# Optimization experiments

Hardware: AMD Instinct MI355X
Metric: run time of the kernel (lower is better)

Reference implementation:

```python
import jax, jax.numpy as jnp
import numpy as np

DIM = 256
NUM_HEADS = 8
SCALE = (DIM // NUM_HEADS) ** -0.5  # matches torch: head_dim**-0.5, even though no head split happens
THRESH = 0.6


def setup_inputs() -> dict:
    key = jax.random.key(0)
    ks = jax.random.split(key, 6)
    B, N = 4, 4096
    x = jax.random.normal(ks[0], (B, N, DIM), dtype=jnp.float32)
    y = jax.random.normal(ks[1], (B, N, DIM), dtype=jnp.float32)
    s = DIM ** -0.5
    Wq = jax.random.normal(ks[2], (DIM, DIM), dtype=jnp.float32) * s
    Wk = jax.random.normal(ks[3], (DIM, DIM), dtype=jnp.float32) * s
    Wv = jax.random.normal(ks[4], (DIM, DIM), dtype=jnp.float32) * s
    Wp = jax.random.normal(ks[5], (DIM, DIM), dtype=jnp.float32) * s
    bp = jnp.zeros((DIM,), dtype=jnp.float32)
    return {"x": x, "y": y, "Wq": Wq, "Wk": Wk, "Wv": Wv, "Wp": Wp, "bp": bp}


def reference(x, y, Wq, Wk, Wv, Wp, bp):
    # q,v from x; k from y (cross attention, no head split — faithful to source)
    q = jnp.einsum('bnd,de->bne', x, Wq)
    k = jnp.einsum('bnd,de->bne', y, Wk)
    v = jnp.einsum('bnd,de->bne', x, Wv)
    attn = jnp.einsum('bnd,bmd->bnm', q, k) * SCALE  # [B, N, N]
    attn = jax.nn.softmax(attn, axis=-1)
    attn = jnp.where(attn < THRESH, jnp.zeros((), attn.dtype), attn)  # hard threshold
    out = jnp.einsum('bnm,bmd->bnd', attn, v)
    out = jnp.einsum('bnd,de->bne', out, Wp) + bp
    return out
```

## Files before the change

### kernel.cpp

```cpp
#include <hip/hip_runtime.h>
#include <cstdint>
#include <cmath>

#define DIM     256
#define NSEQ    4096
#define SCALE   0.17677669529663687f
#define THRESH  0.6f
#define BAND    0.01f
#define MAXSUSP 8000
#define NCHUNK  32
#define C1      0.2550349f
#define C2      28.8539008f

using half8 = __attribute__((ext_vector_type(8))) _Float16;
using half4 = __attribute__((ext_vector_type(4))) _Float16;
using f32x4 = __attribute__((ext_vector_type(4))) float;

__device__ __forceinline__ void async_copy16(const void* gsrc, void* ldst) {
    __builtin_amdgcn_global_load_lds(
        (const __attribute__((address_space(1))) void*)gsrc,
        (__attribute__((address_space(3))) void*)ldst, 16, 0, 0);
}

__global__ void prep_kernel(const float* __restrict__ W0, const float* __restrict__ W1,
                            const float* __restrict__ W2, const float* __restrict__ W3,
                            float* __restrict__ Wt, _Float16* __restrict__ Wth,
                            int* __restrict__ susp)
{
    __shared__ float tile[64][68];
    int t = threadIdx.x;
    int m = blockIdx.x >> 4;
    int ti = blockIdx.x & 15;
    int tr = (ti >> 2) * 64, tc = (ti & 3) * 64;
    const float* W = (m == 0) ? W0 : (m == 1) ? W1 : (m == 2) ? W2 : W3;
    if (blockIdx.x == 0 && t < 2) susp[t] = 0;
    int rr = t >> 4, c4 = (t & 15) * 4;
#pragma unroll
    for (int p = 0; p < 4; ++p) {
        int row = p * 16 + rr;
        *(float4*)&tile[row][c4] = *(const float4*)(W + (size_t)(tr + row) * DIM + tc + c4);
    }
    __syncthreads();
#pragma unroll
    for (int p = 0; p < 4; ++p) {
        int c = p * 16 + rr;
        float4 v;
        v.x = tile[c4 + 0][c]; v.y = tile[c4 + 1][c];
        v.z = tile[c4 + 2][c]; v.w = tile[c4 + 3][c];
        size_t ot = (size_t)(tc + c) * DIM + tr + c4;
        if (m == 0) *(float4*)(Wt + ot) = v;
        half4 hv;
        hv[0] = (_Float16)v.x; hv[1] = (_Float16)v.y;
        hv[2] = (_Float16)v.z; hv[3] = (_Float16)v.w;
        *(half4*)(Wth + (size_t)m * 65536 + ot) = hv;
    }
}

__global__ __launch_bounds__(256, 2)
void proj3_mfma(const float* __restrict__ x, const float* __restrict__ y,
                const _Float16* __restrict__ Wth,
                _Float16* __restrict__ qh, _Float16* __restrict__ kh,
                float* __restrict__ kf, _Float16* __restrict__ vh)
{
    __shared__ half8 sA[1024];
    __shared__ half8 sB[1024];
    int tid = threadIdx.x, w = tid >> 6, ln = tid & 63;
    int rb = blockIdx.x * 128, cb = blockIdx.y * 128, m = blockIdx.z;
    const float* A = (m == 1) ? y : x;
    const _Float16* B = Wth + (size_t)m * 65536;

    f32x4 acc[2][8];
#pragma unroll
    for (int mi = 0; mi < 2; ++mi)
#pragma unroll
        for (int nt = 0; nt < 8; ++nt) acc[mi][nt] = (f32x4){0.f, 0.f, 0.f, 0.f};

    int r = tid >> 1;
    int chalf = (tid & 1) * 4;
    for (int kc = 0; kc < 4; ++kc) {
        __syncthreads();
        const float*    asrc = A + (size_t)(rb + r) * DIM + kc * 64 + chalf * 8;
        const _Float16* bsrc = B + (size_t)(cb + r) * DIM + kc * 64 + chalf * 8;
#pragma unroll
        for (int cc = 0; cc < 4; ++cc) {
            int c = chalf + cc;
            float4 f0 = *(const float4*)(asrc + cc * 8);
            float4 f1 = *(const float4*)(asrc + cc * 8 + 4);
            half8 hv;
            hv[0] = (_Float16)f0.x; hv[1] = (_Float16)f0.y; hv[2] = (_Float16)f0.z; hv[3] = (_Float16)f0.w;
            hv[4] = (_Float16)f1.x; hv[5] = (_Float16)f1.y; hv[6] = (_Float16)f1.z; hv[7] = (_Float16)f1.w;
            int li = ((r >> 4) * 2 + (c >> 2)) * 64 + ((c & 3) << 4) + (r & 15);
            sA[li] = hv;
            sB[li] = *(const half8*)(bsrc + cc * 8);
        }
        __syncthreads();
#pragma unroll
        for (int s = 0; s < 2; ++s) {
            half8 a0 = sA[((w * 2 + 0) * 2 + s) * 64 + ln];
            half8 a1 = sA[((w * 2 + 1) * 2 + s) * 64 + ln];
#pragma unroll
            for (int nt = 0; nt < 8; ++nt) {
                half8 bv = sB[(nt * 2 + s) * 64 + ln];
                acc[0][nt] = __builtin_amdgcn_mfma_f32_16x16x32_f16(a0, bv, acc[0][nt], 0, 0, 0);
                acc[1][nt] = __builtin_amdgcn_mfma_f32_16x16x32_f16(a1, bv, acc[1][nt], 0, 0, 0);
            }
        }
    }
    int quad = ln >> 4, cix = ln & 15;
#pragma unroll
    for (int mi = 0; mi < 2; ++mi)
#pragma unroll
        for (int nt = 0; nt < 8; ++nt)
#pragma unroll
            for (int rr = 0; rr < 4; ++rr) {
                int row = rb + (w * 2 + mi) * 16 + quad * 4 + rr;
                int col = cb + nt * 16 + cix;
                size_t off = (size_t)row * DIM + col;
                float vv = acc[mi][nt][rr];
                if (m == 0)      qh[off] = (_Float16)vv;
                else if (m == 1) { kh[off] = (_Float16)vv; kf[off] = vv; }
                else             vh[off] = (_Float16)vv;
            }
}

__global__ __launch_bounds__(256, 2)
void flash_fp16(const _Float16* __restrict__ qh, const _Float16* __restrict__ kh,
                float* __restrict__ pm, float* __restrict__ pl, int* __restrict__ pam)
{
    __shared__ half8 sK[4096];
    int tid = threadIdx.x, w = tid >> 6, ln = tid & 63;
    int g = blockIdx.x;
    int qt = blockIdx.y;
    int ms = g & 3, b = g >> 2;
    size_t qbase = (size_t)b * NSEQ + qt * 128 + w * 32;
    size_t krow0 = (size_t)b * NSEQ + ms * 1024;
    int ln15 = ln & 15, ln4 = ln >> 4;

    half8 qf[2][8];
#pragma unroll
    for (int mi = 0; mi < 2; ++mi) {
        const _Float16* qsrc = qh + (qbase + mi * 16 + ln15) * DIM + ln4 * 8;
#pragma unroll
        for (int ks = 0; ks < 8; ++ks)
            qf[mi][ks] = *(const half8*)(qsrc + ks * 32);
    }

    float rm[2][4], rl[2][4]; int ram[2][4];
#pragma unroll
    for (int mi = 0; mi < 2; ++mi)
#pragma unroll
        for (int rr = 0; rr < 4; ++rr) { rm[mi][rr] = -INFINITY; rl[mi][rr] = 0.f; ram[mi][rr] = 0; }

    for (int kt = 0; kt < 8; ++kt) {
        __syncthreads();
#pragma unroll
        for (int j = 0; j < 16; ++j) {
            int grp = w * 16 + j;
            int nt = grp >> 3, ks = grp & 7;
            const _Float16* src = kh + (krow0 + kt * 128 + nt * 16 + ln15) * DIM + ks * 32 + ln4 * 8;
            async_copy16(src, (char*)sK + grp * 1024);
        }
        __syncthreads();

        f32x4 acc[2][8];
#pragma unroll
        for (int mi = 0; mi < 2; ++mi)
#pragma unroll
            for (int nt = 0; nt < 8; ++nt) acc[mi][nt] = (f32x4){0.f, 0.f, 0.f, 0.f};

#pragma unroll
        for (int nt = 0; nt < 8; ++nt)
#pragma unroll
            for (int ks = 0; ks < 8; ++ks) {
                half8 bk = sK[(nt * 8 + ks) * 64 + ln];
                acc[0][nt] = __builtin_amdgcn_mfma_f32_16x16x32_f16(qf[0][ks], bk, acc[0][nt], 0, 0, 0);
                acc[1][nt] = __builtin_amdgcn_mfma_f32_16x16x32_f16(qf[1][ks], bk, acc[1][nt], 0, 0, 0);
            }

        int keybase = b * NSEQ + ms * 1024 + kt * 128 + ln15;
#pragma unroll
        for (int mi = 0; mi < 2; ++mi)
#pragma unroll
            for (int rr = 0; rr < 4; ++rr) {
                float mx = rm[mi][rr]; int amx = ram[mi][rr]; float ls = rl[mi][rr];
#pragma unroll
                for (int nt = 0; nt < 8; ++nt) {
                    float a = acc[mi][nt][rr];
                    ls += __builtin_amdgcn_exp2f(fmaf(a, C1, -C2));
                    if (a > mx) { mx = a; amx = keybase + nt * 16; }
                }
                rm[mi][rr] = mx; ram[mi][rr] = amx; rl[mi][rr] = ls;
            }
    }

#pragma unroll
    for (int mi = 0; mi < 2; ++mi)
#pragma unroll
        for (int rr = 0; rr < 4; ++rr) {
            float m0 = rm[mi][rr], l0 = rl[mi][rr]; int am0 = ram[mi][rr];
#pragma unroll
            for (int d = 1; d < 16; d <<= 1) {
                l0 += __shfl_xor(l0, d);
                float m2 = __shfl_xor(m0, d);
                int  am2 = __shfl_xor(am0, d);
                if (m2 > m0) { m0 = m2; am0 = am2; }
            }
            if (ln15 == 0) {
                int row = b * NSEQ + qt * 128 + w * 32 + mi * 16 + ln4 * 4 + rr;
                pm[row * 4 + ms] = m0; pl[row * 4 + ms] = l0; pam[row * 4 + ms] = am0;
            }
        }
}

__global__ void merge_kernel(const float* __restrict__ pm, const float* __restrict__ pl,
                             const int* __restrict__ pam,
                             float* __restrict__ scl, int* __restrict__ sidx,
                             int* __restrict__ susp)
{
    int row = blockIdx.x * 256 + threadIdx.x;
    float m = -INFINITY, l = 0.f; int am = 0;
#pragma unroll
    for (int s = 0; s < 4; ++s) {
        float m2 = pm[row * 4 + s];
        l += pl[row * 4 + s];
        if (m2 > m) { m = m2; am = pam[row * 4 + s]; }
    }
    float p = __builtin_amdgcn_exp2f(fmaf(m, C1, -C2)) / l;
    scl[row] = (p >= THRESH) ? p : 0.f;
    sidx[row] = am;
    if (fabsf(p - THRESH) < BAND) {
        int i = atomicAdd(susp, 1);
        if (i < MAXSUSP) susp[2 + i] = row;
    }
}

__global__ __launch_bounds__(256)
void recheck_q(const float* __restrict__ x, const float* __restrict__ Wtq,
               const int* __restrict__ susp, float* __restrict__ qsusp)
{
    int tid = threadIdx.x;
    int count = susp[0]; if (count > MAXSUSP) count = MAXSUSP;
    for (int i = blockIdx.x; i < count; i += gridDim.x) {
        int row = susp[2 + i];
        const float* xr = x + (size_t)row * DIM;
        const float* wr = Wtq + (size_t)tid * DIM;
        float a = 0.f;
        for (int d = 0; d < DIM; d += 4) {
            float4 xv = *(const float4*)(xr + d);
            float4 wv = *(const float4*)(wr + d);
            a = fmaf(xv.x, wv.x, a); a = fmaf(xv.y, wv.y, a);
            a = fmaf(xv.z, wv.z, a); a = fmaf(xv.w, wv.w, a);
        }
        qsusp[(size_t)i * DIM + tid] = a;
    }
}

__global__ __launch_bounds__(256)
void recheck_part(const float* __restrict__ qsusp, const float* __restrict__ kf,
                  const int* __restrict__ susp,
                  float* __restrict__ pmP, float* __restrict__ plP, int* __restrict__ pamP)
{
    __shared__ float qs[DIM];
    __shared__ float wm[4], wl[4]; __shared__ int wa[4];
    int tid = threadIdx.x;
    int chunk = blockIdx.x;
    int count = susp[0]; if (count > MAXSUSP) count = MAXSUSP;

    for (int i = blockIdx.y; i < count; i += gridDim.y) {
        int row = susp[2 + i];
        int bb = row >> 12;
        __syncthreads();
        qs[tid] = qsusp[(size_t)i * DIM + tid];
        __syncthreads();

        int key = tid >> 1, h = tid & 1;
        int gkey = bb * NSEQ + chunk * 128 + key;
        const float* kr = kf + (size_t)gkey * DIM + h * 128;
        const float* qp = qs + h * 128;
        float dot = 0.f;
#pragma unroll
        for (int j = 0; j < 32; ++j) {
            float4 kv = *(const float4*)(kr + j * 4);
            float4 qv = *(const float4*)(qp + j * 4);
            dot = fmaf(qv.x, kv.x, dot); dot = fmaf(qv.y, kv.y, dot);
            dot = fmaf(qv.z, kv.z, dot); dot = fmaf(qv.w, kv.w, dot);
        }
        dot += __shfl_xor(dot, 1);
        float s = dot * SCALE;

        float m = (h == 0) ? s : -INFINITY;
        float l = (h == 0) ? 1.f : 0.f;
        int  am = (h == 0) ? gkey : 0;
#pragma unroll
        for (int d = 1; d < 64; d <<= 1) {
            float m2 = __shfl_xor(m, d);
            float l2 = __shfl_xor(l, d);
            int  a2 = __shfl_xor(am, d);
            if (m2 > m) { l = l * __expf(m - m2) + l2; m = m2; am = a2; }
            else        { l = l + l2 * __expf(m2 - m); }
        }
        if ((tid & 63) == 0) { wm[tid >> 6] = m; wl[tid >> 6] = l; wa[tid >> 6] = am; }
        __syncthreads();
        if (tid == 0) {
            float M = wm[0], L = wl[0]; int A = wa[0];
#pragma unroll
            for (int wv = 1; wv < 4; ++wv) {
                float m2 = wm[wv], l2 = wl[wv]; int a2 = wa[wv];
                if (m2 > M) { L = L * __expf(M - m2) + l2; M = m2; A = a2; }
                else        { L += l2 * __expf(m2 - M); }
            }
            size_t o = (size_t)i * NCHUNK + chunk;
            pmP[o] = M; plP[o] = L; pamP[o] = A;
        }
    }
}

__global__ __launch_bounds__(256)
void recheck_fold(const float* __restrict__ pmP, const float* __restrict__ plP,
                  const int* __restrict__ pamP, const int* __restrict__ susp,
                  float* __restrict__ scl, int* __restrict__ sidx)
{
    int count = susp[0]; if (count > MAXSUSP) count = MAXSUSP;
    for (int i = blockIdx.x * 256 + threadIdx.x; i < count; i += gridDim.x * 256) {
        float M = -INFINITY, L = 0.f; int A = 0;
#pragma unroll
        for (int c = 0; c < NCHUNK; ++c) {
            size_t o = (size_t)i * NCHUNK + c;
            float m2 = pmP[o], l2 = plP[o]; int a2 = pamP[o];
            if (m2 > M) { L = L * __expf(M - m2) + l2; M = m2; A = a2; }
            else        { L += l2 * __expf(m2 - M); }
        }
        float p = 1.f / L;
        int row = susp[2 + i];
        scl[row] = (p >= THRESH) ? p : 0.f;
        sidx[row] = A;
    }
}

__global__ __launch_bounds__(256, 2)
void out_mfma(const _Float16* __restrict__ vh, const _Float16* __restrict__ Wph,
              const float* __restrict__ scl, const int* __restrict__ sidx,
              const float* __restrict__ bp, float* __restrict__ out)
{
    __shared__ half8 sA[1024];
    __shared__ half8 sB[1024];
    int tid = threadIdx.x, w = tid >> 6, ln = tid & 63;
    int rb = blockIdx.x * 128, cb = blockIdx.y * 128;

    f32x4 acc[2][8];
#pragma unroll
    for (int mi = 0; mi < 2; ++mi)
#pragma unroll
        for (int nt = 0; nt < 8; ++nt) acc[mi][nt] = (f32x4){0.f, 0.f, 0.f, 0.f};

    int r = tid >> 1, chalf = (tid & 1) * 4;
    int gix = sidx[rb + r];
    for (int kc = 0; kc < 4; ++kc) {
        __syncthreads();
        const _Float16* asrc = vh + (size_t)gix * DIM + kc * 64 + chalf * 8;
        const _Float16* bsrc = Wph + (size_t)(cb + r) * DIM + kc * 64 + chalf * 8;
#pragma unroll
        for (int cc = 0; cc < 4; ++cc) {
            int c = chalf + cc;
            int li = ((r >> 4) * 2 + (c >> 2)) * 64 + ((c & 3) << 4) + (r & 15);
            sA[li] = *(const half8*)(asrc + cc * 8);
            sB[li] = *(const half8*)(bsrc + cc * 8);
        }
        __syncthreads();
#pragma unroll
        for (int s = 0; s < 2; ++s) {
            half8 a0 = sA[((w * 2 + 0) * 2 + s) * 64 + ln];
            half8 a1 = sA[((w * 2 + 1) * 2 + s) * 64 + ln];
#pragma unroll
            for (int nt = 0; nt < 8; ++nt) {
                half8 bv = sB[(nt * 2 + s) * 64 + ln];
                acc[0][nt] = __builtin_amdgcn_mfma_f32_16x16x32_f16(a0, bv, acc[0][nt], 0, 0, 0);
                acc[1][nt] = __builtin_amdgcn_mfma_f32_16x16x32_f16(a1, bv, acc[1][nt], 0, 0, 0);
            }
        }
    }
    int quad = ln >> 4, cix = ln & 15;
#pragma unroll
    for (int mi = 0; mi < 2; ++mi)
#pragma unroll
        for (int rr = 0; rr < 4; ++rr) {
            int row = rb + (w * 2 + mi) * 16 + quad * 4 + rr;
            float sc = scl[row];
#pragma unroll
            for (int nt = 0; nt < 8; ++nt) {
                int col = cb + nt * 16 + cix;
                out[(size_t)row * DIM + col] = acc[mi][nt][rr] * sc + bp[col];
            }
        }
}

extern "C" void kernel_launch(void* const* d_in, const int* in_sizes, int n_in,
                              void* d_out, int out_size, void* d_ws, size_t ws_size,
                              hipStream_t stream)
{
    (void)in_sizes; (void)n_in; (void)out_size; (void)ws_size;
    const float* x  = (const float*)d_in[0];
    const float* y  = (const float*)d_in[1];
    const float* Wq = (const float*)d_in[2];
    const float* Wk = (const float*)d_in[3];
    const float* Wv = (const float*)d_in[4];
    const float* Wp = (const float*)d_in[5];
    const float* bp = (const float*)d_in[6];
    float* out = (float*)d_out;

    float* p0 = (float*)d_ws;
    float* kf = p0;                 p0 += 4194304;
    float* Wt = p0;                 p0 += 65536;
    _Float16* Wth = (_Float16*)p0;  p0 += 4 * 65536 / 2;
    _Float16* qh  = (_Float16*)p0;  p0 += 2097152;
    _Float16* kh  = (_Float16*)p0;  p0 += 2097152;
    _Float16* vh  = (_Float16*)p0;  p0 += 2097152;
    float* pm  = p0;                p0 += 65536;
    float* pl  = p0;                p0 += 65536;
    int*  pam  = (int*)p0;          p0 += 65536;
    float* scl = p0;                p0 += 16384;
    int*  sidx = (int*)p0;          p0 += 16384;
    int*  susp = (int*)p0;          p0 += MAXSUSP + 2 + 2;
    float* qsusp = p0;              p0 += (size_t)MAXSUSP * DIM;
    float* pmP = p0;                p0 += (size_t)MAXSUSP * NCHUNK;
    float* plP = p0;                p0 += (size_t)MAXSUSP * NCHUNK;
    int*  pamP = (int*)p0;

    prep_kernel<<<64, 256, 0, stream>>>(Wq, Wk, Wv, Wp, Wt, Wth, susp);
    proj3_mfma<<<dim3(128, 2, 3), 256, 0, stream>>>(x, y, Wth, qh, kh, kf, vh);
    flash_fp16<<<dim3(16, 32), 256, 0, stream>>>(qh, kh, pm, pl, pam);
    merge_kernel<<<64, 256, 0, stream>>>(pm, pl, pam, scl, sidx, susp);
    recheck_q<<<128, 256, 0, stream>>>(x, Wt, susp, qsusp);
    recheck_part<<<dim3(NCHUNK, 64), 256, 0, stream>>>(qsusp, kf, susp, pmP, plP, pamP);
    recheck_fold<<<8, 256, 0, stream>>>(pmP, plP, pamP, susp, scl, sidx);
    out_mfma<<<dim3(128, 2), 256, 0, stream>>>(vh, Wth + 3 * 65536, scl, sidx, bp, out);
}
```

Before: 214.6 us.

## Double-buffer K tiles in flash kernel and load GEMM A operands into registers

The flash score kernel now streams K in 64-key tiles through two LDS buffers. It issues the async copy for the next tile before computing on the current one, which removes one barrier per iteration and overlaps loads with MFMA work. The projection and output GEMMs now load the full 128x256 weight slab into LDS once with async copies. Each wave keeps its A fragments in registers, converted from fp32 or gathered via sidx, instead of going through a staged k-loop. This trades more registers and LDS per block for fewer syncs and fewer LDS round-trips, with some occupancy risk. The flash loop keeps only the barrier at the top of each iteration and issues no explicit wait for the async copy, so it depends on that barrier to make the prefetched tile visible.

```diff
diff --git a/kernel.cpp b/kernel.cpp
--- a/kernel.cpp
+++ b/kernel.cpp
@@ -20,6 +20,15 @@
     __builtin_amdgcn_global_load_lds(
         (const __attribute__((address_space(1))) void*)gsrc,
         (__attribute__((address_space(3))) void*)ldst, 16, 0, 0);
+}
+
+__device__ __forceinline__ half8 cvt8(const float* p) {
+    float4 f0 = *(const float4*)p;
+    float4 f1 = *(const float4*)(p + 4);
+    half8 hv;
+    hv[0] = (_Float16)f0.x; hv[1] = (_Float16)f0.y; hv[2] = (_Float16)f0.z; hv[3] = (_Float16)f0.w;
+    hv[4] = (_Float16)f1.x; hv[5] = (_Float16)f1.y; hv[6] = (_Float16)f1.z; hv[7] = (_Float16)f1.w;
+    return hv;
 }
 
 __global__ void prep_kernel(const float* __restrict__ W0, const float* __restrict__ W1,
@@ -62,12 +71,31 @@
                 _Float16* __restrict__ qh, _Float16* __restrict__ kh,
                 float* __restrict__ kf, _Float16* __restrict__ vh)
 {
-    __shared__ half8 sA[1024];
-    __shared__ half8 sB[1024];
+    __shared__ half8 sB[4096];
     int tid = threadIdx.x, w = tid >> 6, ln = tid & 63;
-    int rb = blockIdx.x * 128, cb = blockIdx.y * 128, m = blockIdx.z;
+    int ln15 = ln & 15, ln4 = ln >> 4;
+    int rb = blockIdx.x * 128, cbh = blockIdx.y, m = blockIdx.z;
     const float* A = (m == 1) ? y : x;
-    const _Float16* B = Wth + (size_t)m * 65536;
+    const _Float16* B = Wth + (size_t)m * 65536 + (size_t)cbh * 128 * DIM;
+
+#pragma unroll
+    for (int j = 0; j < 16; ++j) {
+        int grp = w * 16 + j;
+        int nt = grp >> 3, ks = grp & 7;
+        const _Float16* src = B + (size_t)(nt * 16 + ln15) * DIM + ks * 32 + ln4 * 8;
+        async_copy16(src, (char*)sB + grp * 1024);
+    }
+
+    half8 af[2][8];
+#pragma unroll
+    for (int mi = 0; mi < 2; ++mi) {
+        const float* ar = A + (size_t)(rb + w * 32 + mi * 16 + ln15) * DIM + ln4 * 8;
+#pragma unroll
+        for (int ks = 0; ks < 8; ++ks)
+            af[mi][ks] = cvt8(ar + ks * 32);
+    }
+
+    __syncthreads();
 
     f32x4 acc[2][8];
 #pragma unroll
@@ -75,38 +103,16 @@
 #pragma unroll
         for (int nt = 0; nt < 8; ++nt) acc[mi][nt] = (f32x4){0.f, 0.f, 0.f, 0.f};
 
-    int r = tid >> 1;
-    int chalf = (tid & 1) * 4;
-    for (int kc = 0; kc < 4; ++kc) {
-        __syncthreads();
-        const float*    asrc = A + (size_t)(rb + r) * DIM + kc * 64 + chalf * 8;
-        const _Float16* bsrc = B + (size_t)(cb + r) * DIM + kc * 64 + chalf * 8;
-#pragma unroll
-        for (int cc = 0; cc < 4; ++cc) {
-            int c = chalf + cc;
-            float4 f0 = *(const float4*)(asrc + cc * 8);
-            float4 f1 = *(const float4*)(asrc + cc * 8 + 4);
-            half8 hv;
-            hv[0] = (_Float16)f0.x; hv[1] = (_Float16)f0.y; hv[2] = (_Float16)f0.z; hv[3] = (_Float16)f0.w;
-            hv[4] = (_Float16)f1.x; hv[5] = (_Float16)f1.y; hv[6] = (_Float16)f1.z; hv[7] = (_Float16)f1.w;
-            int li = ((r >> 4) * 2 + (c >> 2)) * 64 + ((c & 3) << 4) + (r & 15);
-            sA[li] = hv;
-            sB[li] = *(const half8*)(bsrc + cc * 8);
-        }
-        __syncthreads();
-#pragma unroll
-        for (int s = 0; s < 2; ++s) {
-            half8 a0 = sA[((w * 2 + 0) * 2 + s) * 64 + ln];
-            half8 a1 = sA[((w * 2 + 1) * 2 + s) * 64 + ln];
-#pragma unroll
-            for (int nt = 0; nt < 8; ++nt) {
-                half8 bv = sB[(nt * 2 + s) * 64 + ln];
-                acc[0][nt] = __builtin_amdgcn_mfma_f32_16x16x32_f16(a0, bv, acc[0][nt], 0, 0, 0);
-                acc[1][nt] = __builtin_amdgcn_mfma_f32_16x16x32_f16(a1, bv, acc[1][nt], 0, 0, 0);
-            }
-        }
-    }
-    int quad = ln >> 4, cix = ln & 15;
+#pragma unroll
+    for (int nt = 0; nt < 8; ++nt)
+#pragma unroll
+        for (int ks = 0; ks < 8; ++ks) {
+            half8 bv = sB[(nt * 8 + ks) * 64 + ln];
+            acc[0][nt] = __builtin_amdgcn_mfma_f32_16x16x32_f16(af[0][ks], bv, acc[0][nt], 0, 0, 0);
+            acc[1][nt] = __builtin_amdgcn_mfma_f32_16x16x32_f16(af[1][ks], bv, acc[1][nt], 0, 0, 0);
+        }
+
+    int quad = ln4, cix = ln15;
 #pragma unroll
     for (int mi = 0; mi < 2; ++mi)
 #pragma unroll
@@ -114,7 +120,7 @@
 #pragma unroll
             for (int rr = 0; rr < 4; ++rr) {
                 int row = rb + (w * 2 + mi) * 16 + quad * 4 + rr;
-                int col = cb + nt * 16 + cix;
+                int col = cbh * 128 + nt * 16 + cix;
                 size_t off = (size_t)row * DIM + col;
                 float vv = acc[mi][nt][rr];
                 if (m == 0)      qh[off] = (_Float16)vv;
@@ -127,7 +133,7 @@
 void flash_fp16(const _Float16* __restrict__ qh, const _Float16* __restrict__ kh,
                 float* __restrict__ pm, float* __restrict__ pl, int* __restrict__ pam)
 {
-    __shared__ half8 sK[4096];
+    __shared__ half8 sK[2][2048];
     int tid = threadIdx.x, w = tid >> 6, ln = tid & 63;
     int g = blockIdx.x;
     int qt = blockIdx.y;
@@ -151,40 +157,51 @@
 #pragma unroll
         for (int rr = 0; rr < 4; ++rr) { rm[mi][rr] = -INFINITY; rl[mi][rr] = 0.f; ram[mi][rr] = 0; }
 
-    for (int kt = 0; kt < 8; ++kt) {
+#pragma unroll
+    for (int j = 0; j < 8; ++j) {
+        int grp = w * 8 + j;
+        const _Float16* src = kh + (krow0 + (grp >> 3) * 16 + ln15) * DIM + (grp & 7) * 32 + ln4 * 8;
+        async_copy16(src, (char*)&sK[0][0] + grp * 1024);
+    }
+
+    for (int kt = 0; kt < 16; ++kt) {
+        int cur = kt & 1;
         __syncthreads();
-#pragma unroll
-        for (int j = 0; j < 16; ++j) {
-            int grp = w * 16 + j;
-            int nt = grp >> 3, ks = grp & 7;
-            const _Float16* src = kh + (krow0 + kt * 128 + nt * 16 + ln15) * DIM + ks * 32 + ln4 * 8;
-            async_copy16(src, (char*)sK + grp * 1024);
-        }
-        __syncthreads();
-
-        f32x4 acc[2][8];
+
+        if (kt + 1 < 16) {
+#pragma unroll
+            for (int j = 0; j < 8; ++j) {
+                int grp = w * 8 + j;
+                const _Float16* src = kh + (krow0 + (kt + 1) * 64 + (grp >> 3) * 16 + ln15) * DIM
+                                      + (grp & 7) * 32 + ln4 * 8;
+                async_copy16(src, (char*)&sK[1 - cur][0] + grp * 1024);
+            }
+        }
+
+        const half8* sKc = &sK[cur][0];
+        f32x4 acc[2][4];
 #pragma unroll
         for (int mi = 0; mi < 2; ++mi)
 #pragma unroll
-            for (int nt = 0; nt < 8; ++nt) acc[mi][nt] = (f32x4){0.f, 0.f, 0.f, 0.f};
-
-#pragma unroll
-        for (int nt = 0; nt < 8; ++nt)
+            for (int nt = 0; nt < 4; ++nt) acc[mi][nt] = (f32x4){0.f, 0.f, 0.f, 0.f};
+
+#pragma unroll
+        for (int nt = 0; nt < 4; ++nt)
 #pragma unroll
             for (int ks = 0; ks < 8; ++ks) {
-                half8 bk = sK[(nt * 8 + ks) * 64 + ln];
+                half8 bk = sKc[(nt * 8 + ks) * 64 + ln];
                 acc[0][nt] = __builtin_amdgcn_mfma_f32_16x16x32_f16(qf[0][ks], bk, acc[0][nt], 0, 0, 0);
                 acc[1][nt] = __builtin_amdgcn_mfma_f32_16x16x32_f16(qf[1][ks], bk, acc[1][nt], 0, 0, 0);
             }
 
-        int keybase = b * NSEQ + ms * 1024 + kt * 128 + ln15;
+        int keybase = b * NSEQ + ms * 1024 + kt * 64 + ln15;
 #pragma unroll
         for (int mi = 0; mi < 2; ++mi)
 #pragma unroll
             for (int rr = 0; rr < 4; ++rr) {
                 float mx = rm[mi][rr]; int amx = ram[mi][rr]; float ls = rl[mi][rr];
 #pragma unroll
-                for (int nt = 0; nt < 8; ++nt) {
+                for (int nt = 0; nt < 4; ++nt) {
                     float a = acc[mi][nt][rr];
                     ls += __builtin_amdgcn_exp2f(fmaf(a, C1, -C2));
                     if (a > mx) { mx = a; amx = keybase + nt * 16; }
@@ -342,10 +359,31 @@
               const float* __restrict__ scl, const int* __restrict__ sidx,
               const float* __restrict__ bp, float* __restrict__ out)
 {
-    __shared__ half8 sA[1024];
-    __shared__ half8 sB[1024];
+    __shared__ half8 sB[4096];
     int tid = threadIdx.x, w = tid >> 6, ln = tid & 63;
-    int rb = blockIdx.x * 128, cb = blockIdx.y * 128;
+    int ln15 = ln & 15, ln4 = ln >> 4;
+    int rb = blockIdx.x * 128, cbh = blockIdx.y;
+    const _Float16* B = Wph + (size_t)cbh * 128 * DIM;
+
+#pragma unroll
+    for (int j = 0; j < 16; ++j) {
+        int grp = w * 16 + j;
+        int nt = grp >> 3, ks = grp & 7;
+        const _Float16* src = B + (size_t)(nt * 16 + ln15) * DIM + ks * 32 + ln4 * 8;
+        async_copy16(src, (char*)sB + grp * 1024);
+    }
+
+    half8 af[2][8];
+#pragma unroll
+    for (int mi = 0; mi < 2; ++mi) {
+        int arow = rb + w * 32 + mi * 16 + ln15;
+        const _Float16* ar = vh + (size_t)sidx[arow] * DIM + ln4 * 8;
+#pragma unroll
+        for (int ks = 0; ks < 8; ++ks)
+            af[mi][ks] = *(const half8*)(ar + ks * 32);
+    }
+
+    __syncthreads();
 
     f32x4 acc[2][8];
 #pragma unroll
@@ -353,33 +391,16 @@
 #pragma unroll
         for (int nt = 0; nt < 8; ++nt) acc[mi][nt] = (f32x4){0.f, 0.f, 0.f, 0.f};
 
-    int r = tid >> 1, chalf = (tid & 1) * 4;
-    int gix = sidx[rb + r];
-    for (int kc = 0; kc < 4; ++kc) {
-        __syncthreads();
-        const _Float16* asrc = vh + (size_t)gix * DIM + kc * 64 + chalf * 8;
-        const _Float16* bsrc = Wph + (size_t)(cb + r) * DIM + kc * 64 + chalf * 8;
-#pragma unroll
-        for (int cc = 0; cc < 4; ++cc) {
-            int c = chalf + cc;
-            int li = ((r >> 4) * 2 + (c >> 2)) * 64 + ((c & 3) << 4) + (r & 15);
-            sA[li] = *(const half8*)(asrc + cc * 8);
-            sB[li] = *(const half8*)(bsrc + cc * 8);
-        }
-        __syncthreads();
-#pragma unroll
-        for (int s = 0; s < 2; ++s) {
-            half8 a0 = sA[((w * 2 + 0) * 2 + s) * 64 + ln];
-            half8 a1 = sA[((w * 2 + 1) * 2 + s) * 64 + ln];
-#pragma unroll
-            for (int nt = 0; nt < 8; ++nt) {
-                half8 bv = sB[(nt * 2 + s) * 64 + ln];
-                acc[0][nt] = __builtin_amdgcn_mfma_f32_16x16x32_f16(a0, bv, acc[0][nt], 0, 0, 0);
-                acc[1][nt] = __builtin_amdgcn_mfma_f32_16x16x32_f16(a1, bv, acc[1][nt], 0, 0, 0);
-            }
-        }
-    }
-    int quad = ln >> 4, cix = ln & 15;
+#pragma unroll
+    for (int nt = 0; nt < 8; ++nt)
+#pragma unroll
+        for (int ks = 0; ks < 8; ++ks) {
+            half8 bv = sB[(nt * 8 + ks) * 64 + ln];
+            acc[0][nt] = __builtin_amdgcn_mfma_f32_16x16x32_f16(af[0][ks], bv, acc[0][nt], 0, 0, 0);
+            acc[1][nt] = __builtin_amdgcn_mfma_f32_16x16x32_f16(af[1][ks], bv, acc[1][nt], 0, 0, 0);
+        }
+
+    int quad = ln4, cix = ln15;
 #pragma unroll
     for (int mi = 0; mi < 2; ++mi)
 #pragma unroll
@@ -388,7 +409,7 @@
             float sc = scl[row];
 #pragma unroll
             for (int nt = 0; nt < 8; ++nt) {
-                int col = cb + nt * 16 + cix;
+                int col = cbh * 128 + nt * 16 + cix;
                 out[(size_t)row * DIM + col] = acc[mi][nt][rr] * sc + bp[col];
             }
         }
```

Result: no change. 210.8 us (-1.8%).
